# Kernel optimization log

Measured on AMD Instinct MI355X. Metric: run time of the kernel, lower is better.

Reference implementation:

```python
import jax, jax.numpy as jnp
import numpy as np

PC_MIN = np.array([-0.5, -0.5, 0.0], dtype=np.float32)
PC_MAX = np.array([0.5, 0.5, 1.0], dtype=np.float32)
VOXEL = 0.025
GRID = 40  # (0.5 - (-0.5)) / 0.025 = 40 per axis
NUM_VOX = GRID * GRID * GRID  # 64000


def setup_inputs() -> dict:
    key = jax.random.key(0)
    k1, k2 = jax.random.split(key)
    B, N, C = 2, 18432, 1024  # N = V*H*W with V=8, H=W=48
    video_features_up = jax.random.normal(k1, (B, N, C), dtype=jnp.float32)
    # points slightly beyond pc_range so some are invalid (masked to zero)
    lo = jnp.array([-0.6, -0.6, -0.1], dtype=jnp.float32)
    hi = jnp.array([0.6, 0.6, 1.1], dtype=jnp.float32)
    u = jax.random.uniform(k2, (B, N, 3), dtype=jnp.float32)
    xyz_down = lo + u * (hi - lo)
    return {"video_features_up": video_features_up, "xyz_down": xyz_down}


def _voxel_ids(xyz):
    # xyz: (B, N, 3) already masked (invalid points set to 0)
    idx = jnp.floor((xyz - jnp.asarray(PC_MIN)) / VOXEL).astype(jnp.int32)
    idx = jnp.clip(idx, 0, GRID - 1)
    return idx[..., 0] + GRID * idx[..., 1] + GRID * GRID * idx[..., 2]  # (B, N)


def reference(video_features_up, xyz_down):
    pc_min = jnp.asarray(PC_MIN)
    pc_max = jnp.asarray(PC_MAX)
    valid = jnp.all((xyz_down > pc_min) & (xyz_down < pc_max), axis=-1)  # (B, N)
    xyz_m = jnp.where(valid[..., None], xyz_down, 0.0)
    feats = jnp.where(valid[..., None], video_features_up, 0.0)
    p2v = _voxel_ids(xyz_m)  # (B, N) int32 in [0, NUM_VOX)

    def pool_one(f, seg):
        sums = jax.ops.segment_sum(f, seg, num_segments=NUM_VOX)  # (NUM_VOX, C)
        cnt = jax.ops.segment_sum(jnp.ones(seg.shape[0], f.dtype), seg,
                                  num_segments=NUM_VOX)
        return sums / jnp.maximum(cnt, 1.0)[:, None]  # scatter_mean

    pooled = jax.vmap(pool_one)(feats, p2v)  # (B, NUM_VOX, C)
    batch_offset = jnp.cumsum(p2v.max(axis=1) + 1).astype(jnp.int32)  # (B,)
    return pooled, batch_offset
```

## Files before the change

kernel.cpp:

```cpp
#include <hip/hip_runtime.h>

constexpr int B  = 2;
constexpr int N  = 18432;
constexpr int C  = 1024;
constexpr int GR = 40;
constexpr int NV = GR * GR * GR;
constexpr int BNV = B * NV;
constexpr int ZERO_VOX = 820;

typedef float v4f __attribute__((ext_vector_type(4)));

__global__ void points_kernel(const float* __restrict__ xyz,
                              int* __restrict__ cntAll,
                              int* __restrict__ head,
                              int* __restrict__ nxt,
                              int* __restrict__ bmax) {
    int i = blockIdx.x * blockDim.x + threadIdx.x;
    int b = i / N;
    int lane = threadIdx.x & 63;

    float x = xyz[3 * i + 0];
    float y = xyz[3 * i + 1];
    float z = xyz[3 * i + 2];

    bool valid = (x > -0.5f) && (x < 0.5f) &&
                 (y > -0.5f) && (y < 0.5f) &&
                 (z >  0.0f) && (z < 1.0f);

    float xm = valid ? x : 0.0f;
    float ym = valid ? y : 0.0f;
    float zm = valid ? z : 0.0f;

    int ix = min(max((int)floorf((xm + 0.5f) / 0.025f), 0), GR - 1);
    int iy = min(max((int)floorf((ym + 0.5f) / 0.025f), 0), GR - 1);
    int iz = min(max((int)floorf(zm / 0.025f), 0), GR - 1);
    int v = ix + GR * iy + GR * GR * iz;

    int m = v;
    #pragma unroll
    for (int o = 32; o >= 1; o >>= 1)
        m = max(m, __shfl_xor(m, o, 64));
    if (lane == 0) atomicMax(&bmax[b], m);

    unsigned long long vb = __ballot(valid);
    int nInv = 64 - __popcll(vb);
    if (lane == 0 && nInv > 0) atomicAdd(&cntAll[b * NV + ZERO_VOX], nInv);

    if (valid) {
        int g = b * NV + v;
        atomicAdd(&cntAll[g], 1);
        nxt[i] = atomicExch(&head[g], i + 1);
    }
}

__global__ void gather_kernel(const float* __restrict__ feats,
                              const int* __restrict__ head,
                              const int* __restrict__ nxt,
                              const int* __restrict__ cntAll,
                              float* __restrict__ out) {
    int g = blockIdx.x;
    int p = head[g];
    float inv = 1.0f / (float)max(cntAll[g], 1);

    v4f acc = {0.0f, 0.0f, 0.0f, 0.0f};
    while (p) {
        int pn = nxt[p - 1];
        const v4f* src = (const v4f*)(feats + (size_t)(p - 1) * C);
        v4f f = src[threadIdx.x];
        acc += f;
        p = pn;
    }
    acc *= inv;
    v4f* dst = (v4f*)(out + (size_t)g * C);
    __builtin_nontemporal_store(acc, dst + threadIdx.x);
}

__global__ void offs_out_kernel(const int* __restrict__ bmax,
                                float* __restrict__ out_offs) {
    if (threadIdx.x == 0 && blockIdx.x == 0) {
        int m0 = bmax[0];
        int m1 = bmax[1];
        out_offs[0] = (float)(m0 + 1);
        out_offs[1] = (float)(m0 + 1 + m1 + 1);
    }
}

extern "C" void kernel_launch(void* const* d_in, const int* in_sizes, int n_in,
                              void* d_out, int out_size, void* d_ws, size_t ws_size,
                              hipStream_t stream) {
    const float* feats = (const float*)d_in[0];
    const float* xyz   = (const float*)d_in[1];
    float* out = (float*)d_out;

    int* w      = (int*)d_ws;
    int* cntAll = w;
    int* head   = cntAll + BNV;
    int* bmax   = head + BNV;
    int* nxt    = bmax + B;

    hipMemsetAsync(cntAll, 0, (size_t)(2 * BNV + B) * sizeof(int), stream);

    points_kernel<<<(B * N) / 256, 256, 0, stream>>>(xyz, cntAll, head, nxt, bmax);
    gather_kernel<<<BNV, 256, 0, stream>>>(feats, head, nxt, cntAll, out);
    offs_out_kernel<<<1, 64, 0, stream>>>(bmax, out + (size_t)B * NV * C);
}
```

Measured before the change: 607.6 us.

## Gather only occupied voxels via worklist and memset-zero the output

Points that first claim a voxel append it to a compact worklist, and the gather kernel processes only listed voxels. Empty voxels are zeroed by a bulk memset of the output instead of one block per voxel. This removes launching and scheduling ~128k blocks whose only job is writing zeros. In exchange it adds a global atomic counter and worklist writes in the point kernel, and scatters output writes. It also shrinks the point kernel blocks to 64 threads.

Result: slower. 624.4 us (+2.8%).

```diff
diff --git a/kernel.cpp b/kernel.cpp
--- a/kernel.cpp
+++ b/kernel.cpp
@@ -14,7 +14,9 @@
                               int* __restrict__ cntAll,
                               int* __restrict__ head,
                               int* __restrict__ nxt,
-                              int* __restrict__ bmax) {
+                              int* __restrict__ bmax,
+                              int* __restrict__ nWork,
+                              int* __restrict__ worklist) {
     int i = blockIdx.x * blockDim.x + threadIdx.x;
     int b = i / N;
     int lane = threadIdx.x & 63;
@@ -49,25 +51,33 @@
     if (valid) {
         int g = b * NV + v;
         atomicAdd(&cntAll[g], 1);
-        nxt[i] = atomicExch(&head[g], i + 1);
+        int old = atomicExch(&head[g], i + 1);
+        nxt[i] = old;
+        if (old == 0) {
+            int slot = atomicAdd(nWork, 1);
+            worklist[slot] = g;
+        }
     }
 }
 
-__global__ void gather_kernel(const float* __restrict__ feats,
+__global__ void gather_sparse(const float* __restrict__ feats,
                               const int* __restrict__ head,
                               const int* __restrict__ nxt,
                               const int* __restrict__ cntAll,
+                              const int* __restrict__ worklist,
+                              const int* __restrict__ nWork,
                               float* __restrict__ out) {
-    int g = blockIdx.x;
+    int e = blockIdx.x;
+    if (e >= *nWork) return;
+    int g = worklist[e];
     int p = head[g];
-    float inv = 1.0f / (float)max(cntAll[g], 1);
+    float inv = 1.0f / (float)cntAll[g];
 
     v4f acc = {0.0f, 0.0f, 0.0f, 0.0f};
     while (p) {
         int pn = nxt[p - 1];
         const v4f* src = (const v4f*)(feats + (size_t)(p - 1) * C);
-        v4f f = src[threadIdx.x];
-        acc += f;
+        acc += src[threadIdx.x];
         p = pn;
     }
     acc *= inv;
@@ -92,15 +102,23 @@
     const float* xyz   = (const float*)d_in[1];
     float* out = (float*)d_out;
 
-    int* w      = (int*)d_ws;
-    int* cntAll = w;
-    int* head   = cntAll + BNV;
-    int* bmax   = head + BNV;
-    int* nxt    = bmax + B;
+    int* w        = (int*)d_ws;
+    int* cntAll   = w;
+    int* head     = cntAll + BNV;
+    int* bmax     = head + BNV;
+    int* nWork    = bmax + B;
+    int* worklist = nWork + 1;
+    int* nxt      = worklist + B * N;
 
-    hipMemsetAsync(cntAll, 0, (size_t)(2 * BNV + B) * sizeof(int), stream);
+    hipMemsetAsync(cntAll, 0, (size_t)(2 * BNV + B + 1) * sizeof(int), stream);
 
-    points_kernel<<<(B * N) / 256, 256, 0, stream>>>(xyz, cntAll, head, nxt, bmax);
-    gather_kernel<<<BNV, 256, 0, stream>>>(feats, head, nxt, cntAll, out);
+    hipMemsetAsync(out, 0, (size_t)B * NV * C * sizeof(float), stream);
+
+    points_kernel<<<(B * N) / 64, 64, 0, stream>>>(xyz, cntAll, head, nxt, bmax,
+                                                   nWork, worklist);
+
+    gather_sparse<<<B * N, 256, 0, stream>>>(feats, head, nxt, cntAll,
+                                             worklist, nWork, out);
+
     offs_out_kernel<<<1, 64, 0, stream>>>(bmax, out + (size_t)B * NV * C);
 }
```

## Process sixteen voxels per wavefront in gather instead of one block per voxel

Applied to the files above, without the earlier changes.

The gather kernel is restructured so each 64-lane wavefront handles 16 consecutive voxels, loading their heads and counts once and broadcasting them with shuffles. Each lane accumulates four float4 slices, so one wave covers a full 1024-channel row. This replaces 128000 tiny blocks, mostly empty voxels that only write zeros, with far fewer blocks, cutting launch and scheduling overhead. The points kernel block size also drops to 64. The risk is less memory-level parallelism per voxel and serialized work inside a wave when some voxels hold many points.

New measurement: 631.9 us. 4.0% more time.

```diff
diff --git a/kernel.cpp b/kernel.cpp
--- a/kernel.cpp
+++ b/kernel.cpp
@@ -7,6 +7,9 @@
 constexpr int NV = GR * GR * GR;
 constexpr int BNV = B * NV;
 constexpr int ZERO_VOX = 820;
+
+constexpr int VPW = 16;
+constexpr int GATHER_BLOCKS = BNV / (4 * VPW);
 
 typedef float v4f __attribute__((ext_vector_type(4)));
 
@@ -53,26 +56,43 @@
     }
 }
 
-__global__ void gather_kernel(const float* __restrict__ feats,
-                              const int* __restrict__ head,
-                              const int* __restrict__ nxt,
-                              const int* __restrict__ cntAll,
-                              float* __restrict__ out) {
-    int g = blockIdx.x;
-    int p = head[g];
-    float inv = 1.0f / (float)max(cntAll[g], 1);
+__global__ __launch_bounds__(256) void gather_dense(const float* __restrict__ feats,
+                                                    const int* __restrict__ head,
+                                                    const int* __restrict__ nxt,
+                                                    const int* __restrict__ cntAll,
+                                                    float* __restrict__ out) {
+    int waveId = blockIdx.x * (blockDim.x >> 6) + (threadIdx.x >> 6);
+    int lane   = threadIdx.x & 63;
+    int gBase  = waveId * VPW;
+    if (gBase >= BNV) return;
 
-    v4f acc = {0.0f, 0.0f, 0.0f, 0.0f};
-    while (p) {
-        int pn = nxt[p - 1];
-        const v4f* src = (const v4f*)(feats + (size_t)(p - 1) * C);
-        v4f f = src[threadIdx.x];
-        acc += f;
-        p = pn;
+    int hv = 0;
+    if (lane < VPW)                 hv = head[gBase + lane];
+    int cv = 0;
+    if (lane >= VPW && lane < 2*VPW) cv = cntAll[gBase + (lane - VPW)];
+
+    for (int k = 0; k < VPW; ++k) {
+        int p = __shfl(hv, k, 64);
+        v4f a0{0,0,0,0}, a1{0,0,0,0}, a2{0,0,0,0}, a3{0,0,0,0};
+        if (p) {
+            float inv = 1.0f / (float)__shfl(cv, VPW + k, 64);
+            while (p) {
+                int pn = nxt[p - 1];
+                const v4f* src = (const v4f*)(feats + (size_t)(p - 1) * C);
+                a0 += src[lane];
+                a1 += src[lane + 64];
+                a2 += src[lane + 128];
+                a3 += src[lane + 192];
+                p = pn;
+            }
+            a0 *= inv; a1 *= inv; a2 *= inv; a3 *= inv;
+        }
+        v4f* dst = (v4f*)(out + (size_t)(gBase + k) * C);
+        __builtin_nontemporal_store(a0, dst + lane);
+        __builtin_nontemporal_store(a1, dst + lane + 64);
+        __builtin_nontemporal_store(a2, dst + lane + 128);
+        __builtin_nontemporal_store(a3, dst + lane + 192);
     }
-    acc *= inv;
-    v4f* dst = (v4f*)(out + (size_t)g * C);
-    __builtin_nontemporal_store(acc, dst + threadIdx.x);
 }
 
 __global__ void offs_out_kernel(const int* __restrict__ bmax,
@@ -100,7 +120,9 @@
 
     hipMemsetAsync(cntAll, 0, (size_t)(2 * BNV + B) * sizeof(int), stream);
 
-    points_kernel<<<(B * N) / 256, 256, 0, stream>>>(xyz, cntAll, head, nxt, bmax);
-    gather_kernel<<<BNV, 256, 0, stream>>>(feats, head, nxt, cntAll, out);
+    points_kernel<<<(B * N) / 64, 64, 0, stream>>>(xyz, cntAll, head, nxt, bmax);
+
+    gather_dense<<<GATHER_BLOCKS, 256, 0, stream>>>(feats, head, nxt, cntAll, out);
+
     offs_out_kernel<<<1, 64, 0, stream>>>(bmax, out + (size_t)B * NV * C);
 }
```
